# Optimization experiments

Hardware: AMD Instinct MI355X
Metric: run time of the kernel (lower is better)

Reference implementation:

```python
import jax, jax.numpy as jnp
import numpy as np

T, B, D_IN, H = 512, 256, 128, 256


def setup_inputs() -> dict:
    key = jax.random.key(0)
    k1, k2, k3, k4, k5 = jax.random.split(key, 5)
    s_ih = 1.0 / np.sqrt(H)
    return {
        "inputs": jax.random.normal(k1, (T, B, D_IN), dtype=jnp.float32),
        "W_ih": jax.random.normal(k2, (4 * H, D_IN), dtype=jnp.float32) * s_ih,
        "W_hh": jax.random.normal(k3, (4 * H, H), dtype=jnp.float32) * s_ih,
        "b_ih": jax.random.normal(k4, (4 * H,), dtype=jnp.float32) * s_ih,
        "b_hh": jax.random.normal(k5, (4 * H,), dtype=jnp.float32) * s_ih,
    }


def reference(inputs, W_ih, W_hh, b_ih, b_hh):
    # LSTM recurrence over time, PyTorch LSTMCell gate order: i, f, g, o.
    hidden = W_hh.shape[1]
    # Precompute input projections for all timesteps: [T, B, 4H]
    x_proj = jnp.einsum('tbd,gd->tbg', inputs, W_ih) + b_ih + b_hh

    def step(carry, xp):
        h, c = carry
        gates = xp + h @ W_hh.T  # [B, 4H]
        i, f, g, o = jnp.split(gates, 4, axis=-1)
        i = jax.nn.sigmoid(i)
        f = jax.nn.sigmoid(f)
        g = jnp.tanh(g)
        o = jax.nn.sigmoid(o)
        c_new = f * c + i * g
        h_new = o * jnp.tanh(c_new)
        return (h_new, c_new), h_new

    B_ = inputs.shape[1]
    h0 = jnp.zeros((B_, hidden), dtype=inputs.dtype)
    c0 = jnp.zeros((B_, hidden), dtype=inputs.dtype)
    _, outputs = jax.lax.scan(step, (h0, c0), x_proj)
    return outputs  # [T, B, H]
```

## Files before the change

kernel.cpp:

```cpp
#include <hip/hip_runtime.h>
#include <stddef.h>

#define T_STEPS 512
#define BATCH   256
#define DIN     128
#define HID     256
#define HXS     392

typedef __attribute__((ext_vector_type(8))) short  short8;
typedef __attribute__((ext_vector_type(4))) float  floatx4;

__device__ __forceinline__ unsigned short f2bf(float f) {
    unsigned u = __builtin_bit_cast(unsigned, f);
    u += 0x7FFFu + ((u >> 16) & 1u);
    return (unsigned short)(u >> 16);
}
__device__ __forceinline__ short8 pack8(floatx4 a, floatx4 b) {
    short8 r;
    r[0]=(short)f2bf(a[0]); r[1]=(short)f2bf(a[1]); r[2]=(short)f2bf(a[2]); r[3]=(short)f2bf(a[3]);
    r[4]=(short)f2bf(b[0]); r[5]=(short)f2bf(b[1]); r[6]=(short)f2bf(b[2]); r[7]=(short)f2bf(b[3]);
    return r;
}
__device__ __forceinline__ float sigmoid_f(float x) { return 1.0f / (1.0f + __expf(-x)); }
__device__ __forceinline__ float tanh_f(float x) {
    float e = __expf(-2.0f * fabsf(x));
    float r = (1.0f - e) / (1.0f + e);
    return copysignf(r, x);
}

__global__ void __launch_bounds__(256, 2) lstm_persistent(
    const float* __restrict__ x_in,
    const float* __restrict__ W_ih,
    const float* __restrict__ W_hh,
    const float* __restrict__ b_ih,
    const float* __restrict__ b_hh,
    float*               __restrict__ out,
    unsigned long long*  __restrict__ xch)
{
    __shared__ unsigned short hx[16][HXS];
    __shared__ float gbuf[4][16][20];

    const int tid  = threadIdx.x;
    const int lane = tid & 63;
    const int wave = tid >> 6;
    const int quad = lane >> 4;
    const int l16  = lane & 15;

    const int bx = blockIdx.x;
    const int g  = (bx & 7) * 2 + ((bx >> 3) & 1);
    const int m  = bx >> 4;

    short8 wfrag[12];
    {
        const int r = wave * 256 + m * 16 + l16;
        const float* wh = W_hh + (size_t)r * HID;
        const float* wi = W_ih + (size_t)r * DIN;
#pragma unroll
        for (int kt = 0; kt < 8; ++kt) {
            floatx4 a = *(const floatx4*)(wh + kt * 32 + quad * 8);
            floatx4 b = *(const floatx4*)(wh + kt * 32 + quad * 8 + 4);
            wfrag[kt] = pack8(a, b);
        }
#pragma unroll
        for (int kt = 8; kt < 12; ++kt) {
            floatx4 a = *(const floatx4*)(wi + (kt - 8) * 32 + quad * 8);
            floatx4 b = *(const floatx4*)(wi + (kt - 8) * 32 + quad * 8 + 4);
            wfrag[kt] = pack8(a, b);
        }
    }

    const int tb = tid >> 4;
    const int tc = tid & 15;
    const int grow = g * 16 + tb;
    float bias[4];
#pragma unroll
    for (int gi = 0; gi < 4; ++gi) {
        int r = gi * 256 + m * 16 + tc;
        bias[gi] = b_ih[r] + b_hh[r];
    }
    float c_state = 0.0f;

#pragma unroll
    for (int j = 0; j < 16; ++j) hx[tb][tc * 16 + j] = 0;
    {
        const float* src = x_in + (size_t)grow * DIN + tc * 8;
        floatx4 a = *(const floatx4*)src;
        floatx4 b = *(const floatx4*)(src + 4);
        *(short8*)&hx[tb][256 + tc * 8] = pack8(a, b);
    }
    __syncthreads();

    for (int t = 1; t <= T_STEPS; ++t) {
        short8 afrag[12];
#pragma unroll
        for (int kt = 0; kt < 12; ++kt)
            afrag[kt] = *(const short8*)&hx[l16][kt * 32 + quad * 8];

        floatx4 acc0 = {0.f, 0.f, 0.f, 0.f};
        floatx4 acc1 = {0.f, 0.f, 0.f, 0.f};
#pragma unroll
        for (int kt = 0; kt < 12; kt += 2) {
            acc0 = __builtin_amdgcn_mfma_f32_16x16x32_bf16(afrag[kt],     wfrag[kt],     acc0, 0, 0, 0);
            acc1 = __builtin_amdgcn_mfma_f32_16x16x32_bf16(afrag[kt + 1], wfrag[kt + 1], acc1, 0, 0, 0);
        }
        floatx4 acc = acc0 + acc1;

#pragma unroll
        for (int r = 0; r < 4; ++r)
            gbuf[wave][quad * 4 + r][l16] = acc[r];
        __syncthreads();

        float iv = sigmoid_f(gbuf[0][tb][tc] + bias[0]);
        float fv = sigmoid_f(gbuf[1][tb][tc] + bias[1]);
        float gv = tanh_f   (gbuf[2][tb][tc] + bias[2]);
        float ov = sigmoid_f(gbuf[3][tb][tc] + bias[3]);
        c_state = fv * c_state + iv * gv;
        float hv = ov * tanh_f(c_state);

        __builtin_nontemporal_store(hv, out + ((size_t)(t - 1) * BATCH + grow) * HID + m * 16 + tc);

        if (t < T_STEPS) {
            unsigned short hu = f2bf(hv);
            unsigned short hn = (unsigned short)__shfl_xor((int)hu, 1, 64);
            if ((tc & 1) == 0) {
                unsigned long long w = ((unsigned long long)(unsigned)t << 32)
                                     | (unsigned)hu | ((unsigned)hn << 16);
                size_t widx = (((size_t)(t & 1) * BATCH) + grow) * (HID / 2) + (m * 8 + (tc >> 1));
                __hip_atomic_store(&xch[widx], w, __ATOMIC_RELAXED, __HIP_MEMORY_SCOPE_AGENT);
            }
            __atomic_signal_fence(__ATOMIC_SEQ_CST);

            {
                const float* src = x_in + ((size_t)t * BATCH + grow) * DIN + tc * 8;
                floatx4 a = *(const floatx4*)src;
                floatx4 b = *(const floatx4*)(src + 4);
                *(short8*)&hx[tb][256 + tc * 8] = pack8(a, b);
            }

            size_t rbase = (((size_t)(t & 1) * BATCH) + grow) * (HID / 2) + tc * 8;
            unsigned long long v[8];
            for (;;) {
                bool ok = true;
#pragma unroll
                for (int i = 0; i < 8; ++i) {
                    v[i] = __hip_atomic_load(&xch[rbase + i],
                                             __ATOMIC_RELAXED, __HIP_MEMORY_SCOPE_AGENT);
                    ok &= ((unsigned)(v[i] >> 32) == (unsigned)t);
                }
                if (ok) break;
            }
            short8 h0, h1;
#pragma unroll
            for (int i = 0; i < 4; ++i) {
                h0[2 * i]     = (short)(v[i] & 0xFFFF);
                h0[2 * i + 1] = (short)((v[i] >> 16) & 0xFFFF);
                h1[2 * i]     = (short)(v[i + 4] & 0xFFFF);
                h1[2 * i + 1] = (short)((v[i + 4] >> 16) & 0xFFFF);
            }
            *(short8*)&hx[tb][tc * 16]     = h0;
            *(short8*)&hx[tb][tc * 16 + 8] = h1;
        }
        __syncthreads();
    }
}

extern "C" void kernel_launch(void* const* d_in, const int* in_sizes, int n_in,
                              void* d_out, int out_size, void* d_ws, size_t ws_size,
                              hipStream_t stream) {
    const float* x   = (const float*)d_in[0];
    const float* wih = (const float*)d_in[1];
    const float* whh = (const float*)d_in[2];
    const float* bih = (const float*)d_in[3];
    const float* bhh = (const float*)d_in[4];
    unsigned long long* xch = (unsigned long long*)d_ws;

    hipLaunchKernelGGL(lstm_persistent, dim3(256), dim3(256), 0, stream,
                       x, wih, whh, bih, bhh, (float*)d_out, xch);
}
```

Baseline: 1.229 ms.

## Repartition LSTM across 64 blocks of 512 threads with local h reuse

Work is split across 64 persistent blocks of 512 threads instead of 256 blocks of 256 threads. Each block now owns 64 hidden columns for its batch group, and each wave runs two MFMA tiles per step, so fewer blocks take part in the cross-block exchange. Each block writes its own h slice straight into shared memory and only spin-polls the 192 foreign columns, and the next x load is issued before the matmul. The cost is more weight registers per thread and more serial MFMA work per block on the critical path, set against less global atomic traffic and less synchronization fan-in.

```diff
diff --git a/kernel.cpp b/kernel.cpp
--- a/kernel.cpp
+++ b/kernel.cpp
@@ -6,9 +6,12 @@
 #define DIN     128
 #define HID     256
 #define HXS     392
+#define GBS     72
 
 typedef __attribute__((ext_vector_type(8))) short  short8;
+typedef __attribute__((ext_vector_type(4))) short  bf16x4;
 typedef __attribute__((ext_vector_type(4))) float  floatx4;
+typedef __attribute__((ext_vector_type(2))) float  floatx2;
 
 __device__ __forceinline__ unsigned short f2bf(float f) {
     unsigned u = __builtin_bit_cast(unsigned, f);
@@ -21,14 +24,25 @@
     r[4]=(short)f2bf(b[0]); r[5]=(short)f2bf(b[1]); r[6]=(short)f2bf(b[2]); r[7]=(short)f2bf(b[3]);
     return r;
 }
+__device__ __forceinline__ bf16x4 pack4(floatx4 a) {
+    bf16x4 r;
+    r[0]=(short)f2bf(a[0]); r[1]=(short)f2bf(a[1]);
+    r[2]=(short)f2bf(a[2]); r[3]=(short)f2bf(a[3]);
+    return r;
+}
 __device__ __forceinline__ float sigmoid_f(float x) { return 1.0f / (1.0f + __expf(-x)); }
 __device__ __forceinline__ float tanh_f(float x) {
     float e = __expf(-2.0f * fabsf(x));
     float r = (1.0f - e) / (1.0f + e);
     return copysignf(r, x);
 }
+__device__ __forceinline__ int foreign_pair(int fp, int mp) {
+    int j = fp >> 5, o = fp & 31;
+    int mm = j + (j >= mp ? 1 : 0);
+    return mm * 32 + o;
+}
 
-__global__ void __launch_bounds__(256, 2) lstm_persistent(
+__global__ void __launch_bounds__(512, 2) lstm_persistent(
     const float* __restrict__ x_in,
     const float* __restrict__ W_ih,
     const float* __restrict__ W_hh,
@@ -38,7 +52,7 @@
     unsigned long long*  __restrict__ xch)
 {
     __shared__ unsigned short hx[16][HXS];
-    __shared__ float gbuf[4][16][20];
+    __shared__ float gbuf[4][16][GBS];
 
     const int tid  = threadIdx.x;
     const int lane = tid & 63;
@@ -46,119 +60,125 @@
     const int quad = lane >> 4;
     const int l16  = lane & 15;
 
-    const int bx = blockIdx.x;
-    const int g  = (bx & 7) * 2 + ((bx >> 3) & 1);
-    const int m  = bx >> 4;
+    const int g  = blockIdx.x >> 2;
+    const int mp = blockIdx.x & 3;
 
-    short8 wfrag[12];
+    const int gw   = wave >> 1;
+    const int half = wave & 1;
+
+    short8 wfrag0[12], wfrag1[12];
     {
-        const int r = wave * 256 + m * 16 + l16;
-        const float* wh = W_hh + (size_t)r * HID;
-        const float* wi = W_ih + (size_t)r * DIN;
+        const int r0 = gw * 256 + mp * 64 + half * 32 + l16;
+        const int r1 = r0 + 16;
+        const float* wh0 = W_hh + (size_t)r0 * HID;
+        const float* wi0 = W_ih + (size_t)r0 * DIN;
+        const float* wh1 = W_hh + (size_t)r1 * HID;
+        const float* wi1 = W_ih + (size_t)r1 * DIN;
 #pragma unroll
         for (int kt = 0; kt < 8; ++kt) {
-            floatx4 a = *(const floatx4*)(wh + kt * 32 + quad * 8);
-            floatx4 b = *(const floatx4*)(wh + kt * 32 + quad * 8 + 4);
-            wfrag[kt] = pack8(a, b);
+            wfrag0[kt] = pack8(*(const floatx4*)(wh0 + kt * 32 + quad * 8),
+                               *(const floatx4*)(wh0 + kt * 32 + quad * 8 + 4));
+            wfrag1[kt] = pack8(*(const floatx4*)(wh1 + kt * 32 + quad * 8),
+                               *(const floatx4*)(wh1 + kt * 32 + quad * 8 + 4));
         }
 #pragma unroll
         for (int kt = 8; kt < 12; ++kt) {
-            floatx4 a = *(const floatx4*)(wi + (kt - 8) * 32 + quad * 8);
-            floatx4 b = *(const floatx4*)(wi + (kt - 8) * 32 + quad * 8 + 4);
-            wfrag[kt] = pack8(a, b);
+            wfrag0[kt] = pack8(*(const floatx4*)(wi0 + (kt - 8) * 32 + quad * 8),
+                               *(const floatx4*)(wi0 + (kt - 8) * 32 + quad * 8 + 4));
+            wfrag1[kt] = pack8(*(const floatx4*)(wi1 + (kt - 8) * 32 + quad * 8),
+                               *(const floatx4*)(wi1 + (kt - 8) * 32 + quad * 8 + 4));
         }
     }
 
-    const int tb = tid >> 4;
-    const int tc = tid & 15;
+    const int tb   = tid >> 5;
+    const int tc2  = tid & 31;
     const int grow = g * 16 + tb;
-    float bias[4];
+    const int lc   = 2 * tc2;
+    const int c0   = mp * 64 + lc;
+
+    float bias[4][2];
 #pragma unroll
-    for (int gi = 0; gi < 4; ++gi) {
-        int r = gi * 256 + m * 16 + tc;
-        bias[gi] = b_ih[r] + b_hh[r];
+    for (int q = 0; q < 4; ++q) {
+        int r = q * 256 + c0;
+        bias[q][0] = b_ih[r] + b_hh[r];
+        bias[q][1] = b_ih[r + 1] + b_hh[r + 1];
     }
-    float c_state = 0.0f;
+    float cs0 = 0.f, cs1 = 0.f;
 
-#pragma unroll
-    for (int j = 0; j < 16; ++j) hx[tb][tc * 16 + j] = 0;
+    const int gp0 = foreign_pair(tc2 * 3,     mp);
+    const int gp1 = foreign_pair(tc2 * 3 + 1, mp);
+    const int gp2 = foreign_pair(tc2 * 3 + 2, mp);
+    unsigned long long* const xrow = xch + (size_t)grow * (HID / 2);
+
+    *(short8*)&hx[tb][tc2 * 8] = (short8){0, 0, 0, 0, 0, 0, 0, 0};
     {
-        const float* src = x_in + (size_t)grow * DIN + tc * 8;
-        floatx4 a = *(const floatx4*)src;
-        floatx4 b = *(const floatx4*)(src + 4);
-        *(short8*)&hx[tb][256 + tc * 8] = pack8(a, b);
+        floatx4 x0 = *(const floatx4*)(x_in + (size_t)grow * DIN + tc2 * 4);
+        *(bf16x4*)&hx[tb][256 + tc2 * 4] = pack4(x0);
     }
     __syncthreads();
 
     for (int t = 1; t <= T_STEPS; ++t) {
-        short8 afrag[12];
-#pragma unroll
-        for (int kt = 0; kt < 12; ++kt)
-            afrag[kt] = *(const short8*)&hx[l16][kt * 32 + quad * 8];
+        const unsigned tag = (unsigned)t;
+
+        floatx4 xv = {0.f, 0.f, 0.f, 0.f};
+        if (t < T_STEPS)
+            xv = *(const floatx4*)(x_in + ((size_t)t * BATCH + grow) * DIN + tc2 * 4);
 
         floatx4 acc0 = {0.f, 0.f, 0.f, 0.f};
         floatx4 acc1 = {0.f, 0.f, 0.f, 0.f};
 #pragma unroll
-        for (int kt = 0; kt < 12; kt += 2) {
-            acc0 = __builtin_amdgcn_mfma_f32_16x16x32_bf16(afrag[kt],     wfrag[kt],     acc0, 0, 0, 0);
-            acc1 = __builtin_amdgcn_mfma_f32_16x16x32_bf16(afrag[kt + 1], wfrag[kt + 1], acc1, 0, 0, 0);
+        for (int kt = 0; kt < 12; ++kt) {
+            short8 a = *(const short8*)&hx[l16][kt * 32 + quad * 8];
+            acc0 = __builtin_amdgcn_mfma_f32_16x16x32_bf16(a, wfrag0[kt], acc0, 0, 0, 0);
+            acc1 = __builtin_amdgcn_mfma_f32_16x16x32_bf16(a, wfrag1[kt], acc1, 0, 0, 0);
         }
-        floatx4 acc = acc0 + acc1;
-
 #pragma unroll
-        for (int r = 0; r < 4; ++r)
-            gbuf[wave][quad * 4 + r][l16] = acc[r];
+        for (int r = 0; r < 4; ++r) {
+            gbuf[gw][quad * 4 + r][half * 32 + l16]      = acc0[r];
+            gbuf[gw][quad * 4 + r][half * 32 + 16 + l16] = acc1[r];
+        }
         __syncthreads();
 
-        float iv = sigmoid_f(gbuf[0][tb][tc] + bias[0]);
-        float fv = sigmoid_f(gbuf[1][tb][tc] + bias[1]);
-        float gv = tanh_f   (gbuf[2][tb][tc] + bias[2]);
-        float ov = sigmoid_f(gbuf[3][tb][tc] + bias[3]);
-        c_state = fv * c_state + iv * gv;
-        float hv = ov * tanh_f(c_state);
-
-        __builtin_nontemporal_store(hv, out + ((size_t)(t - 1) * BATCH + grow) * HID + m * 16 + tc);
+        floatx2 gI = *(const floatx2*)&gbuf[0][tb][lc];
+        floatx2 gF = *(const floatx2*)&gbuf[1][tb][lc];
+        floatx2 gG = *(const floatx2*)&gbuf[2][tb][lc];
+        floatx2 gO = *(const floatx2*)&gbuf[3][tb][lc];
+        float i0 = sigmoid_f(gI[0] + bias[0][0]), i1 = sigmoid_f(gI[1] + bias[0][1]);
+        float f0 = sigmoid_f(gF[0] + bias[1][0]), f1 = sigmoid_f(gF[1] + bias[1][1]);
+        float g0 = tanh_f   (gG[0] + bias[2][0]), g1 = tanh_f   (gG[1] + bias[2][1]);
+        float o0 = sigmoid_f(gO[0] + bias[3][0]), o1 = sigmoid_f(gO[1] + bias[3][1]);
+        cs0 = f0 * cs0 + i0 * g0;
+        cs1 = f1 * cs1 + i1 * g1;
+        float hv0 = o0 * tanh_f(cs0);
+        float hv1 = o1 * tanh_f(cs1);
 
         if (t < T_STEPS) {
-            unsigned short hu = f2bf(hv);
-            unsigned short hn = (unsigned short)__shfl_xor((int)hu, 1, 64);
-            if ((tc & 1) == 0) {
-                unsigned long long w = ((unsigned long long)(unsigned)t << 32)
-                                     | (unsigned)hu | ((unsigned)hn << 16);
-                size_t widx = (((size_t)(t & 1) * BATCH) + grow) * (HID / 2) + (m * 8 + (tc >> 1));
-                __hip_atomic_store(&xch[widx], w, __ATOMIC_RELAXED, __HIP_MEMORY_SCOPE_AGENT);
-            }
+            unsigned pay = (unsigned)f2bf(hv0) | ((unsigned)f2bf(hv1) << 16);
+            unsigned long long wrd = ((unsigned long long)tag << 32) | pay;
+            unsigned long long* bp = xrow + (size_t)(t & 1) * (BATCH * (HID / 2));
+            __hip_atomic_store(&bp[mp * 32 + tc2], wrd, __ATOMIC_RELAXED, __HIP_MEMORY_SCOPE_AGENT);
             __atomic_signal_fence(__ATOMIC_SEQ_CST);
 
-            {
-                const float* src = x_in + ((size_t)t * BATCH + grow) * DIN + tc * 8;
-                floatx4 a = *(const floatx4*)src;
-                floatx4 b = *(const floatx4*)(src + 4);
-                *(short8*)&hx[tb][256 + tc * 8] = pack8(a, b);
+            floatx2 ho = {hv0, hv1};
+            __builtin_nontemporal_store(ho, (floatx2*)(out + ((size_t)(t - 1) * BATCH + grow) * HID + c0));
+
+            *(bf16x4*)&hx[tb][256 + tc2 * 4] = pack4(xv);
+            *(unsigned*)&hx[tb][c0] = pay;
+
+            unsigned long long v0, v1, v2;
+            for (;;) {
+                v0 = __hip_atomic_load(&bp[gp0], __ATOMIC_RELAXED, __HIP_MEMORY_SCOPE_AGENT);
+                v1 = __hip_atomic_load(&bp[gp1], __ATOMIC_RELAXED, __HIP_MEMORY_SCOPE_AGENT);
+                v2 = __hip_atomic_load(&bp[gp2], __ATOMIC_RELAXED, __HIP_MEMORY_SCOPE_AGENT);
+                if (((unsigned)(v0 >> 32) == tag) & ((unsigned)(v1 >> 32) == tag)
+                  & ((unsigned)(v2 >> 32) == tag)) break;
             }
-
-            size_t rbase = (((size_t)(t & 1) * BATCH) + grow) * (HID / 2) + tc * 8;
-            unsigned long long v[8];
-            for (;;) {
-                bool ok = true;
-#pragma unroll
-                for (int i = 0; i < 8; ++i) {
-                    v[i] = __hip_atomic_load(&xch[rbase + i],
-                                             __ATOMIC_RELAXED, __HIP_MEMORY_SCOPE_AGENT);
-                    ok &= ((unsigned)(v[i] >> 32) == (unsigned)t);
-                }
-                if (ok) break;
-            }
-            short8 h0, h1;
-#pragma unroll
-            for (int i = 0; i < 4; ++i) {
-                h0[2 * i]     = (short)(v[i] & 0xFFFF);
-                h0[2 * i + 1] = (short)((v[i] >> 16) & 0xFFFF);
-                h1[2 * i]     = (short)(v[i + 4] & 0xFFFF);
-                h1[2 * i + 1] = (short)((v[i + 4] >> 16) & 0xFFFF);
-            }
-            *(short8*)&hx[tb][tc * 16]     = h0;
-            *(short8*)&hx[tb][tc * 16 + 8] = h1;
+            *(unsigned*)&hx[tb][2 * gp0] = (unsigned)v0;
+            *(unsigned*)&hx[tb][2 * gp1] = (unsigned)v1;
+            *(unsigned*)&hx[tb][2 * gp2] = (unsigned)v2;
+        } else {
+            floatx2 ho = {hv0, hv1};
+            __builtin_nontemporal_store(ho, (floatx2*)(out + ((size_t)(t - 1) * BATCH + grow) * HID + c0));
         }
         __syncthreads();
     }
@@ -174,6 +194,6 @@
     const float* bhh = (const float*)d_in[4];
     unsigned long long* xch = (unsigned long long*)d_ws;
 
-    hipLaunchKernelGGL(lstm_persistent, dim3(256), dim3(256), 0, stream,
+    hipLaunchKernelGGL(lstm_persistent, dim3(64), dim3(512), 0, stream,
                        x, wih, whh, bih, bhh, (float*)d_out, xch);
 }
```

Measured after the change: 1.428 ms. +16.2%, slower.

## Interleave two batch halves per block to hide cross-block hidden-state exchange latency

Applied to the files above, without the earlier changes.

Each persistent block now owns two 16-row batch groups (A and B) and alternates between them. While one group's hidden state is being exchanged through global memory with the other blocks, the block computes the other group's step. The grid shrinks from 256 to 128 blocks, and per-block work per step doubles, trading parallelism for hidden synchronization latency. Sigmoid and tanh also switch to the hardware reciprocal approximation instead of a full division.

```diff
diff --git a/kernel.cpp b/kernel.cpp
--- a/kernel.cpp
+++ b/kernel.cpp
@@ -21,11 +21,51 @@
     r[4]=(short)f2bf(b[0]); r[5]=(short)f2bf(b[1]); r[6]=(short)f2bf(b[2]); r[7]=(short)f2bf(b[3]);
     return r;
 }
-__device__ __forceinline__ float sigmoid_f(float x) { return 1.0f / (1.0f + __expf(-x)); }
+__device__ __forceinline__ float sigmoid_f(float x) {
+    return __builtin_amdgcn_rcpf(1.0f + __expf(-x));
+}
 __device__ __forceinline__ float tanh_f(float x) {
     float e = __expf(-2.0f * fabsf(x));
-    float r = (1.0f - e) / (1.0f + e);
+    float r = (1.0f - e) * __builtin_amdgcn_rcpf(1.0f + e);
     return copysignf(r, x);
+}
+__device__ __forceinline__ float lstm_cell(float a0, float a1, float a2, float a3,
+                                           const float* bias, float& cst) {
+    float iv = sigmoid_f(a0 + bias[0]);
+    float fv = sigmoid_f(a1 + bias[1]);
+    float gv = tanh_f   (a2 + bias[2]);
+    float ov = sigmoid_f(a3 + bias[3]);
+    cst = fv * cst + iv * gv;
+    return ov * tanh_f(cst);
+}
+__device__ __forceinline__ void issue_poll(const unsigned long long* p, unsigned long long* v) {
+#pragma unroll
+    for (int i = 0; i < 8; ++i)
+        v[i] = __hip_atomic_load(&p[i], __ATOMIC_RELAXED, __HIP_MEMORY_SCOPE_AGENT);
+}
+__device__ __forceinline__ void finish_poll(const unsigned long long* p, unsigned tag,
+                                            unsigned long long* v) {
+    for (;;) {
+        bool ok = true;
+#pragma unroll
+        for (int i = 0; i < 8; ++i) ok &= ((unsigned)(v[i] >> 32) == tag);
+        if (ok) return;
+#pragma unroll
+        for (int i = 0; i < 8; ++i)
+            v[i] = __hip_atomic_load(&p[i], __ATOMIC_RELAXED, __HIP_MEMORY_SCOPE_AGENT);
+    }
+}
+__device__ __forceinline__ void scatter_h(const unsigned long long* v, unsigned short* dst) {
+    short8 h0, h1;
+#pragma unroll
+    for (int i = 0; i < 4; ++i) {
+        h0[2 * i]     = (short)(v[i] & 0xFFFF);
+        h0[2 * i + 1] = (short)((v[i] >> 16) & 0xFFFF);
+        h1[2 * i]     = (short)(v[i + 4] & 0xFFFF);
+        h1[2 * i + 1] = (short)((v[i + 4] >> 16) & 0xFFFF);
+    }
+    *(short8*)dst       = h0;
+    *(short8*)(dst + 8) = h1;
 }
 
 __global__ void __launch_bounds__(256, 2) lstm_persistent(
@@ -37,7 +77,8 @@
     float*               __restrict__ out,
     unsigned long long*  __restrict__ xch)
 {
-    __shared__ unsigned short hx[16][HXS];
+    __shared__ unsigned short hxA[16][HXS];
+    __shared__ unsigned short hxB[16][HXS];
     __shared__ float gbuf[4][16][20];
 
     const int tid  = threadIdx.x;
@@ -46,9 +87,8 @@
     const int quad = lane >> 4;
     const int l16  = lane & 15;
 
-    const int bx = blockIdx.x;
-    const int g  = (bx & 7) * 2 + ((bx >> 3) & 1);
-    const int m  = bx >> 4;
+    const int m = blockIdx.x >> 3;
+    const int g = blockIdx.x & 7;
 
     short8 wfrag[12];
     {
@@ -56,109 +96,134 @@
         const float* wh = W_hh + (size_t)r * HID;
         const float* wi = W_ih + (size_t)r * DIN;
 #pragma unroll
-        for (int kt = 0; kt < 8; ++kt) {
-            floatx4 a = *(const floatx4*)(wh + kt * 32 + quad * 8);
-            floatx4 b = *(const floatx4*)(wh + kt * 32 + quad * 8 + 4);
-            wfrag[kt] = pack8(a, b);
-        }
-#pragma unroll
-        for (int kt = 8; kt < 12; ++kt) {
-            floatx4 a = *(const floatx4*)(wi + (kt - 8) * 32 + quad * 8);
-            floatx4 b = *(const floatx4*)(wi + (kt - 8) * 32 + quad * 8 + 4);
-            wfrag[kt] = pack8(a, b);
-        }
-    }
-
-    const int tb = tid >> 4;
-    const int tc = tid & 15;
-    const int grow = g * 16 + tb;
+        for (int kt = 0; kt < 8; ++kt)
+            wfrag[kt] = pack8(*(const floatx4*)(wh + kt * 32 + quad * 8),
+                              *(const floatx4*)(wh + kt * 32 + quad * 8 + 4));
+#pragma unroll
+        for (int kt = 8; kt < 12; ++kt)
+            wfrag[kt] = pack8(*(const floatx4*)(wi + (kt - 8) * 32 + quad * 8),
+                              *(const floatx4*)(wi + (kt - 8) * 32 + quad * 8 + 4));
+    }
+
+    const int tb   = tid >> 4;
+    const int tc   = tid & 15;
+    const size_t rowA = (size_t)g * 16 + tb;
+    const size_t rowB = 128 + (size_t)g * 16 + tb;
     float bias[4];
 #pragma unroll
     for (int gi = 0; gi < 4; ++gi) {
         int r = gi * 256 + m * 16 + tc;
         bias[gi] = b_ih[r] + b_hh[r];
     }
-    float c_state = 0.0f;
-
-#pragma unroll
-    for (int j = 0; j < 16; ++j) hx[tb][tc * 16 + j] = 0;
+    float cstA = 0.0f, cstB = 0.0f;
+
+#pragma unroll
+    for (int j = 0; j < 16; ++j) { hxA[tb][tc * 16 + j] = 0; hxB[tb][tc * 16 + j] = 0; }
     {
-        const float* src = x_in + (size_t)grow * DIN + tc * 8;
-        floatx4 a = *(const floatx4*)src;
-        floatx4 b = *(const floatx4*)(src + 4);
-        *(short8*)&hx[tb][256 + tc * 8] = pack8(a, b);
+        const float* sA = x_in + rowA * DIN + tc * 8;
+        const float* sB = x_in + rowB * DIN + tc * 8;
+        *(short8*)&hxA[tb][256 + tc * 8] = pack8(*(const floatx4*)sA, *(const floatx4*)(sA + 4));
+        *(short8*)&hxB[tb][256 + tc * 8] = pack8(*(const floatx4*)sB, *(const floatx4*)(sB + 4));
     }
     __syncthreads();
 
     for (int t = 1; t <= T_STEPS; ++t) {
-        short8 afrag[12];
-#pragma unroll
-        for (int kt = 0; kt < 12; ++kt)
-            afrag[kt] = *(const short8*)&hx[l16][kt * 32 + quad * 8];
-
-        floatx4 acc0 = {0.f, 0.f, 0.f, 0.f};
-        floatx4 acc1 = {0.f, 0.f, 0.f, 0.f};
-#pragma unroll
-        for (int kt = 0; kt < 12; kt += 2) {
-            acc0 = __builtin_amdgcn_mfma_f32_16x16x32_bf16(afrag[kt],     wfrag[kt],     acc0, 0, 0, 0);
-            acc1 = __builtin_amdgcn_mfma_f32_16x16x32_bf16(afrag[kt + 1], wfrag[kt + 1], acc1, 0, 0, 0);
-        }
-        floatx4 acc = acc0 + acc1;
-
-#pragma unroll
-        for (int r = 0; r < 4; ++r)
-            gbuf[wave][quad * 4 + r][l16] = acc[r];
-        __syncthreads();
-
-        float iv = sigmoid_f(gbuf[0][tb][tc] + bias[0]);
-        float fv = sigmoid_f(gbuf[1][tb][tc] + bias[1]);
-        float gv = tanh_f   (gbuf[2][tb][tc] + bias[2]);
-        float ov = sigmoid_f(gbuf[3][tb][tc] + bias[3]);
-        c_state = fv * c_state + iv * gv;
-        float hv = ov * tanh_f(c_state);
-
-        __builtin_nontemporal_store(hv, out + ((size_t)(t - 1) * BATCH + grow) * HID + m * 16 + tc);
-
-        if (t < T_STEPS) {
-            unsigned short hu = f2bf(hv);
-            unsigned short hn = (unsigned short)__shfl_xor((int)hu, 1, 64);
-            if ((tc & 1) == 0) {
-                unsigned long long w = ((unsigned long long)(unsigned)t << 32)
-                                     | (unsigned)hu | ((unsigned)hn << 16);
-                size_t widx = (((size_t)(t & 1) * BATCH) + grow) * (HID / 2) + (m * 8 + (tc >> 1));
-                __hip_atomic_store(&xch[widx], w, __ATOMIC_RELAXED, __HIP_MEMORY_SCOPE_AGENT);
+        const unsigned tag = (unsigned)t;
+        const bool last = (t == T_STEPS);
+        unsigned long long* slotCur  = xch + (size_t)(t & 1)       * (BATCH * (HID / 2));
+        unsigned long long* slotPrev = xch + (size_t)((t - 1) & 1) * (BATCH * (HID / 2));
+
+        unsigned long long pvB[8];
+        const unsigned long long* pB = slotPrev + rowB * (HID / 2) + tc * 8;
+        if (t > 1) issue_poll(pB, pvB);
+
+        floatx4 xa0 = {0,0,0,0}, xa1 = {0,0,0,0}, xb0 = {0,0,0,0}, xb1 = {0,0,0,0};
+        if (!last) {
+            const float* sA = x_in + ((size_t)t * BATCH + rowA) * DIN + tc * 8;
+            const float* sB = x_in + ((size_t)t * BATCH + rowB) * DIN + tc * 8;
+            xa0 = *(const floatx4*)sA; xa1 = *(const floatx4*)(sA + 4);
+            xb0 = *(const floatx4*)sB; xb1 = *(const floatx4*)(sB + 4);
+        }
+
+        {
+            floatx4 acc0 = {0,0,0,0}, acc1 = {0,0,0,0};
+#pragma unroll
+            for (int kt = 0; kt < 12; kt += 2) {
+                short8 a0 = *(const short8*)&hxA[l16][kt * 32 + quad * 8];
+                short8 a1 = *(const short8*)&hxA[l16][(kt + 1) * 32 + quad * 8];
+                acc0 = __builtin_amdgcn_mfma_f32_16x16x32_bf16(a0, wfrag[kt],     acc0, 0, 0, 0);
+                acc1 = __builtin_amdgcn_mfma_f32_16x16x32_bf16(a1, wfrag[kt + 1], acc1, 0, 0, 0);
+            }
+            floatx4 acc = acc0 + acc1;
+#pragma unroll
+            for (int r = 0; r < 4; ++r) gbuf[wave][quad * 4 + r][l16] = acc[r];
+        }
+        __syncthreads();
+
+        {
+            float hvA = lstm_cell(gbuf[0][tb][tc], gbuf[1][tb][tc],
+                                  gbuf[2][tb][tc], gbuf[3][tb][tc], bias, cstA);
+            __builtin_nontemporal_store(hvA, out + ((size_t)(t - 1) * BATCH + rowA) * HID + m * 16 + tc);
+            if (!last) {
+                unsigned short hu = f2bf(hvA);
+                unsigned short hn = (unsigned short)__shfl_xor((int)hu, 1, 64);
+                if ((tc & 1) == 0) {
+                    unsigned long long w = ((unsigned long long)tag << 32)
+                                         | (unsigned)hu | ((unsigned)hn << 16);
+                    __hip_atomic_store(&slotCur[rowA * (HID / 2) + m * 8 + (tc >> 1)], w,
+                                       __ATOMIC_RELAXED, __HIP_MEMORY_SCOPE_AGENT);
+                }
             }
             __atomic_signal_fence(__ATOMIC_SEQ_CST);
-
-            {
-                const float* src = x_in + ((size_t)t * BATCH + grow) * DIN + tc * 8;
-                floatx4 a = *(const floatx4*)src;
-                floatx4 b = *(const floatx4*)(src + 4);
-                *(short8*)&hx[tb][256 + tc * 8] = pack8(a, b);
-            }
-
-            size_t rbase = (((size_t)(t & 1) * BATCH) + grow) * (HID / 2) + tc * 8;
-            unsigned long long v[8];
-            for (;;) {
-                bool ok = true;
-#pragma unroll
-                for (int i = 0; i < 8; ++i) {
-                    v[i] = __hip_atomic_load(&xch[rbase + i],
-                                             __ATOMIC_RELAXED, __HIP_MEMORY_SCOPE_AGENT);
-                    ok &= ((unsigned)(v[i] >> 32) == (unsigned)t);
+        }
+
+        if (t > 1) {
+            finish_poll(pB, tag - 1, pvB);
+            scatter_h(pvB, &hxB[tb][tc * 16]);
+        }
+        __syncthreads();
+
+        unsigned long long pvA[8];
+        const unsigned long long* pA = slotCur + rowA * (HID / 2) + tc * 8;
+        if (!last) issue_poll(pA, pvA);
+
+        {
+            floatx4 acc0 = {0,0,0,0}, acc1 = {0,0,0,0};
+#pragma unroll
+            for (int kt = 0; kt < 12; kt += 2) {
+                short8 a0 = *(const short8*)&hxB[l16][kt * 32 + quad * 8];
+                short8 a1 = *(const short8*)&hxB[l16][(kt + 1) * 32 + quad * 8];
+                acc0 = __builtin_amdgcn_mfma_f32_16x16x32_bf16(a0, wfrag[kt],     acc0, 0, 0, 0);
+                acc1 = __builtin_amdgcn_mfma_f32_16x16x32_bf16(a1, wfrag[kt + 1], acc1, 0, 0, 0);
+            }
+            floatx4 acc = acc0 + acc1;
+#pragma unroll
+            for (int r = 0; r < 4; ++r) gbuf[wave][quad * 4 + r][l16] = acc[r];
+        }
+        __syncthreads();
+
+        {
+            float hvB = lstm_cell(gbuf[0][tb][tc], gbuf[1][tb][tc],
+                                  gbuf[2][tb][tc], gbuf[3][tb][tc], bias, cstB);
+            __builtin_nontemporal_store(hvB, out + ((size_t)(t - 1) * BATCH + rowB) * HID + m * 16 + tc);
+            if (!last) {
+                unsigned short hu = f2bf(hvB);
+                unsigned short hn = (unsigned short)__shfl_xor((int)hu, 1, 64);
+                if ((tc & 1) == 0) {
+                    unsigned long long w = ((unsigned long long)tag << 32)
+                                         | (unsigned)hu | ((unsigned)hn << 16);
+                    __hip_atomic_store(&slotCur[rowB * (HID / 2) + m * 8 + (tc >> 1)], w,
+                                       __ATOMIC_RELAXED, __HIP_MEMORY_SCOPE_AGENT);
                 }
-                if (ok) break;
-            }
-            short8 h0, h1;
-#pragma unroll
-            for (int i = 0; i < 4; ++i) {
-                h0[2 * i]     = (short)(v[i] & 0xFFFF);
-                h0[2 * i + 1] = (short)((v[i] >> 16) & 0xFFFF);
-                h1[2 * i]     = (short)(v[i + 4] & 0xFFFF);
-                h1[2 * i + 1] = (short)((v[i + 4] >> 16) & 0xFFFF);
-            }
-            *(short8*)&hx[tb][tc * 16]     = h0;
-            *(short8*)&hx[tb][tc * 16 + 8] = h1;
+            }
+            __atomic_signal_fence(__ATOMIC_SEQ_CST);
+        }
+
+        if (!last) {
+            finish_poll(pA, tag, pvA);
+            scatter_h(pvA, &hxA[tb][tc * 16]);
+            *(short8*)&hxA[tb][256 + tc * 8] = pack8(xa0, xa1);
+            *(short8*)&hxB[tb][256 + tc * 8] = pack8(xb0, xb1);
         }
         __syncthreads();
     }
@@ -174,6 +239,6 @@
     const float* bhh = (const float*)d_in[4];
     unsigned long long* xch = (unsigned long long*)d_ws;
 
-    hipLaunchKernelGGL(lstm_persistent, dim3(256), dim3(256), 0, stream,
+    hipLaunchKernelGGL(lstm_persistent, dim3(128), dim3(256), 0, stream,
                        x, wih, whh, bih, bhh, (float*)d_out, xch);
 }
```

Result: slower. 1.869 ms (+52.1%).
